# Kernel optimization log

Hardware: AMD Instinct MI355X
Metric: run time of the kernel (lower is better)

## Reference

```python
import jax, jax.numpy as jnp
import numpy as np

B, S, D, H = 2, 2048, 1024, 16
HD = D // H  # 64


def setup_inputs() -> dict:
    key = jax.random.key(0)
    ks = jax.random.split(key, 11)
    w_scale = 1.0 / np.sqrt(D)
    Q = jax.random.normal(ks[0], (B, S, D), jnp.float32)
    K = jax.random.normal(ks[1], (B, S, D), jnp.float32)
    V = jax.random.normal(ks[2], (B, S, D), jnp.float32)
    # causal mask: True = masked (matches torch masked_fill semantics)
    mask = ~jnp.tril(jnp.ones((S, S), bool))[None, None]  # [1,1,S,S]
    # RoPE freqs (precomputed cos/sin of freqs_cis, shape [S, HD//2])
    inv_freq = 1.0 / (10000.0 ** (jnp.arange(0, HD, 2, dtype=jnp.float32) / HD))
    angles = jnp.arange(S, dtype=jnp.float32)[:, None] * inv_freq[None, :]
    freqs_cos, freqs_sin = jnp.cos(angles), jnp.sin(angles)
    wq = jax.random.normal(ks[3], (D, D), jnp.float32) * w_scale
    wk = jax.random.normal(ks[4], (D, D), jnp.float32) * w_scale
    wv = jax.random.normal(ks[5], (D, D), jnp.float32) * w_scale
    wo = jax.random.normal(ks[6], (D, D), jnp.float32) * w_scale
    bq = jax.random.normal(ks[7], (D,), jnp.float32) * 0.01
    bk = jax.random.normal(ks[8], (D,), jnp.float32) * 0.01
    bv = jax.random.normal(ks[9], (D,), jnp.float32) * 0.01
    bo = jax.random.normal(ks[10], (D,), jnp.float32) * 0.01
    return {"Q": Q, "K": K, "V": V, "mask": mask,
            "freqs_cos": freqs_cos, "freqs_sin": freqs_sin,
            "wq": wq, "bq": bq, "wk": wk, "bk": bk,
            "wv": wv, "bv": bv, "wo": wo, "bo": bo}


def _rope(x, cos, sin):
    # x: [B,S,H,HD]; complex pairing of adjacent dims as in view_as_complex
    xr, xi = x[..., 0::2], x[..., 1::2]
    c = cos[None, :, None, :]
    s = sin[None, :, None, :]
    out_r = xr * c - xi * s
    out_i = xr * s + xi * c
    return jnp.stack([out_r, out_i], axis=-1).reshape(x.shape)


def reference(Q, K, V, mask, freqs_cos, freqs_sin, wq, bq, wk, bk, wv, bv, wo, bo):
    b, s, d = Q.shape
    h = H
    hd = d // h
    q = (Q @ wq.T + bq).reshape(b, s, h, hd)
    k = (K @ wk.T + bk).reshape(b, s, h, hd)
    v = (V @ wv.T + bv).reshape(b, s, h, hd)
    q = _rope(q, freqs_cos, freqs_sin)
    k = _rope(k, freqs_cos, freqs_sin)
    q = q.transpose(0, 2, 1, 3)  # [B,H,S,HD]
    k = k.transpose(0, 2, 1, 3)
    v = v.transpose(0, 2, 1, 3)
    scale = jnp.sqrt(jnp.float32(hd))
    energy = jnp.einsum('bhqd,bhkd->bhqk', q, k) / scale
    energy = jnp.where(mask, jnp.float32(-1e10), energy)
    attn = jax.nn.softmax(energy, axis=-1)  # dropout p=0.0 -> identity
    out = jnp.einsum('bhqk,bhkd->bhqd', attn, v)
    out = out.transpose(0, 2, 1, 3).reshape(b, s, d)
    return out @ wo.T + bo
```

## Files before the change

kernel.cpp:

```cpp
#include <hip/hip_runtime.h>
#include <stdint.h>

#define NB 2
#define NS 2048
#define ND 1024
#define NH 16
#define NHD 64
#define NM (NB*NS)

typedef __bf16 bf16;
typedef float f32x4 __attribute__((ext_vector_type(4)));
typedef __bf16 bf16x8 __attribute__((ext_vector_type(8)));
typedef __bf16 bf16x4 __attribute__((ext_vector_type(4)));

#define MFMA16(a,b,c) __builtin_amdgcn_mfma_f32_16x16x32_bf16(a,b,c,0,0,0)

__device__ __forceinline__ void gld_lds16(const bf16* g, bf16* l) {
  __builtin_amdgcn_global_load_lds((const __attribute__((address_space(1))) void*)g,
                                   (__attribute__((address_space(3))) void*)l,
                                   16, 0, 0);
}

__device__ __forceinline__ void block_sync_lds() {
  asm volatile("s_waitcnt lgkmcnt(0)\n\ts_barrier" ::: "memory");
}

__global__ __launch_bounds__(256)
void cvt3(const float* __restrict__ s0, const float* __restrict__ s1,
          const float* __restrict__ s2, bf16* __restrict__ dst, int n4each) {
  const int t = blockIdx.y;
  const float* s = (t == 0) ? s0 : (t == 1) ? s1 : s2;
  int i = blockIdx.x * blockDim.x + threadIdx.x;
  if (i >= n4each) return;
  float4 v = ((const float4*)s)[i];
  bf16x4 o = { (bf16)v.x, (bf16)v.y, (bf16)v.z, (bf16)v.w };
  ((bf16x4*)(dst + (size_t)t * n4each * 4))[i] = o;
}

__global__ __launch_bounds__(256)
void cvt_w4(const float* __restrict__ s0, const float* __restrict__ s1,
            const float* __restrict__ s2, const float* __restrict__ s3,
            bf16* __restrict__ dst, int n4each) {
  const int t = blockIdx.y;
  const float* s = (t == 0) ? s0 : (t == 1) ? s1 : (t == 2) ? s2 : s3;
  int i = blockIdx.x * blockDim.x + threadIdx.x;
  if (i >= n4each) return;
  float4 v = ((const float4*)s)[i];
  bf16x4 o = { (bf16)v.x, (bf16)v.y, (bf16)v.z, (bf16)v.w };
  ((bf16x4*)(dst + (size_t)t * n4each * 4))[i] = o;
}

template<int MODE>
__global__ __launch_bounds__(256)
void gemm_nt(const bf16* __restrict__ A, const bf16* __restrict__ W,
             const float* __restrict__ b0, const float* __restrict__ b1,
             const float* __restrict__ b2,
             const float* __restrict__ fc, const float* __restrict__ fs,
             bf16* __restrict__ obf, bf16* __restrict__ vtp,
             float* __restrict__ of) {
  constexpr int K = ND;
  constexpr int BN = (MODE == 0) ? 128 : 64;
  constexpr int NJ = (MODE == 0) ? 4 : 2;
  constexpr int ITB = (MODE == 0) ? 4 : 2;
  __shared__ __align__(16) bf16 As[128 * 64];
  __shared__ __align__(16) bf16 Bs[BN * 64];
  const int tid = threadIdx.x;
  const int w = tid >> 6, lane = tid & 63;

  const int id = blockIdx.x;
  const int xcd = id & 7, r = id >> 3;
  int t, nt, mt;
  if (MODE == 0) { t = r >> 5; const int rem = r & 31; nt = rem & 7;  mt = xcd + 8 * (rem >> 3); }
  else           { t = 0;                              nt = r & 15;   mt = xcd + 8 * (r >> 4);   }

  const bf16* Ab = A + (size_t)t * ((size_t)NM * K);
  const bf16* Wb = W + (size_t)t * ((size_t)ND * K);
  const float* bias = (t == 0) ? b0 : (t == 1) ? b1 : b2;
  const int wr = (w >> 1) * 64, wc = (w & 1) * (BN / 2);
  f32x4 acc[4][NJ] = {};

  const int swsrc = (((lane & 7) ^ ((lane >> 3) & 7)) << 3);
  const bf16* ga = Ab + (size_t)(mt * 128 + w * 8 + (lane >> 3)) * K + swsrc;
  const bf16* gb = Wb + (size_t)(nt * BN + w * 8 + (lane >> 3)) * K + swsrc;

  for (int k0 = 0; k0 < K; k0 += 64) {
    __syncthreads();
#pragma unroll
    for (int it = 0; it < 4; ++it)
      gld_lds16(ga + (size_t)(it * 32) * K + k0, As + (it * 4 + w) * 512);
#pragma unroll
    for (int it = 0; it < ITB; ++it)
      gld_lds16(gb + (size_t)(it * 32) * K + k0, Bs + (it * 4 + w) * 512);
    __syncthreads();

#pragma unroll
    for (int ks = 0; ks < 2; ++ks) {
      bf16x8 af[4], bfr[NJ];
#pragma unroll
      for (int i = 0; i < 4; ++i) {
        const int row = wr + i * 16 + (lane & 15);
        af[i] = *(const bf16x8*)&As[row * 64 +
                 (((ks * 4 + (lane >> 4)) ^ (lane & 7)) << 3)];
      }
#pragma unroll
      for (int j = 0; j < NJ; ++j) {
        const int row = wc + j * 16 + (lane & 15);
        bfr[j] = *(const bf16x8*)&Bs[row * 64 +
                  (((ks * 4 + (lane >> 4)) ^ (lane & 7)) << 3)];
      }
#pragma unroll
      for (int i = 0; i < 4; ++i)
#pragma unroll
        for (int j = 0; j < NJ; ++j)
          acc[i][j] = MFMA16(af[i], bfr[j], acc[i][j]);
    }
  }

#pragma unroll
  for (int i = 0; i < 4; ++i) {
#pragma unroll
    for (int j = 0; j < NJ; ++j) {
      const int gcol = nt * BN + wc + j * 16 + (lane & 15);
      const float bv = bias[gcol];
      if (MODE == 0 && t == 2) {
        const int s0g = mt * 128 + wr + i * 16 + (lane >> 4) * 4;
        const int b = s0g >> 11, s = s0g & (NS - 1);
        const int h = gcol >> 6, hd = gcol & 63;
        bf16x4 pk = { (bf16)(acc[i][j][0] + bv), (bf16)(acc[i][j][1] + bv),
                      (bf16)(acc[i][j][2] + bv), (bf16)(acc[i][j][3] + bv) };
        *(bf16x4*)&vtp[((size_t)(b * NH + h) * NHD + hd) * NS + s] = pk;
        continue;
      }
#pragma unroll
      for (int r4 = 0; r4 < 4; ++r4) {
        const int grow = mt * 128 + wr + i * 16 + (lane >> 4) * 4 + r4;
        float v = acc[i][j][r4] + bv;
        if (MODE == 0) {
          const int b = grow >> 11, s = grow & (NS - 1);
          const int h = gcol >> 6, hd = gcol & 63;
          float pv = __shfl_xor(v, 1);
          const int ii = hd >> 1;
          float c  = fc[(s << 5) + ii];
          float sn = fs[(s << 5) + ii];
          v = ((hd & 1) == 0) ? (v * c - pv * sn) : (pv * sn + v * c);
          if (t == 0) v *= 0.18033688011112042f;
          obf[(size_t)t * ((size_t)NM * ND) +
              (((size_t)(b * NH + h) * NS + s) * NHD + hd)] = (bf16)v;
        } else {
          of[(size_t)grow * ND + gcol] = v;
        }
      }
    }
  }
}

__device__ __forceinline__ void attn_tile(
    const bf16* __restrict__ Ksh, const bf16* __restrict__ Vsh,
    bf16* __restrict__ Pw, const bf16x8* qf, f32x4* o,
    float& m, float& l, int qi, int kk0, bool diag, int qrow, int grp) {
  const int s7 = qrow & 7;
  f32x4 sc[4] = {};
  __builtin_amdgcn_s_setprio(1);
#pragma unroll
  for (int ch = 0; ch < 2; ++ch)
#pragma unroll
    for (int cb = 0; cb < 4; ++cb) {
      bf16x8 kf = *(const bf16x8*)
        &Ksh[(cb * 16 + qrow) * 64 + (((ch * 4 + grp) ^ s7) << 3)];
      sc[cb] = MFMA16(kf, qf[ch], sc[cb]);
    }
  __builtin_amdgcn_s_setprio(0);

  if (diag) {
#pragma unroll
    for (int cb = 0; cb < 4; ++cb)
#pragma unroll
      for (int r = 0; r < 4; ++r)
        if (kk0 + cb * 16 + grp * 4 + r > qi) sc[cb][r] = -1e30f;
  }

  float a0 = fmaxf(fmaxf(sc[0][0], sc[0][1]), fmaxf(sc[0][2], sc[0][3]));
  float a1 = fmaxf(fmaxf(sc[1][0], sc[1][1]), fmaxf(sc[1][2], sc[1][3]));
  float a2 = fmaxf(fmaxf(sc[2][0], sc[2][1]), fmaxf(sc[2][2], sc[2][3]));
  float a3 = fmaxf(fmaxf(sc[3][0], sc[3][1]), fmaxf(sc[3][2], sc[3][3]));
  float pm = fmaxf(fmaxf(a0, a1), fmaxf(a2, a3));

  if (__any(pm > m + 8.f)) {
    float px = fmaxf(pm, __shfl_xor(pm, 16));
    px = fmaxf(px, __shfl_xor(px, 32));
    const float mn = fmaxf(m, px);
    const float scl = exp2f(m - mn);
    m = mn;
    l *= scl;
#pragma unroll
    for (int hb = 0; hb < 4; ++hb)
#pragma unroll
      for (int r = 0; r < 4; ++r) o[hb][r] *= scl;
  }

#pragma unroll
  for (int cb = 0; cb < 4; ++cb) {
    bf16x4 pk;
#pragma unroll
    for (int r = 0; r < 4; ++r) {
      float p = exp2f(sc[cb][r] - m);
      l += p;
      pk[r] = (bf16)p;
    }
    *(bf16x4*)&Pw[qrow * 64 + (((((cb << 1) | (grp >> 1)) ^ s7) << 3)) +
                  ((grp & 1) << 2)] = pk;
  }

  __builtin_amdgcn_s_setprio(1);
#pragma unroll
  for (int ch = 0; ch < 2; ++ch) {
    bf16x8 pa = *(const bf16x8*)
      &Pw[qrow * 64 + (((ch * 4 + grp) ^ s7) << 3)];
#pragma unroll
    for (int hb = 0; hb < 4; ++hb) {
      bf16x8 vf = *(const bf16x8*)
        &Vsh[(hb * 16 + qrow) * 64 + (((ch * 4 + grp) ^ s7) << 3)];
      o[hb] = MFMA16(vf, pa, o[hb]);
    }
  }
  __builtin_amdgcn_s_setprio(0);
}

__global__ __launch_bounds__(512, 4)
void attn_k(const bf16* __restrict__ q, const bf16* __restrict__ k,
            const bf16* __restrict__ vt, bf16* __restrict__ out) {
  __shared__ __align__(16) char smem[81920];
  bf16* KV = (bf16*)smem;
  bf16* Pr = (bf16*)(smem + 65536);
  auto MO = (float(*)[2][16][68])smem;
  auto ML = (float(*)[2][16][2])(smem + 36864);

  const int tid = threadIdx.x;
  const int w = tid >> 6, lane = tid & 63;
  const int h = w >> 2, wl = w & 3;
  const int qrow = lane & 15, grp = lane >> 4;
  const int bh = blockIdx.x, j = blockIdx.y;
  const int b = bh >> 4, hh = bh & (NH - 1);
  const int tA = j, tB = 31 - j;

  const bf16* qb = q + (size_t)bh * NS * NHD;
  const bf16* kb = k + (size_t)bh * NS * NHD;
  const bf16* vb = vt + (size_t)bh * NHD * NS;

  const int nA = (j >= h) ? (((j - h) >> 1) + 1) : 0;
  const int nB = (((31 - j) - h) >> 1) + 1;
  const int len = nA + nB;

  const int q0A = tA * 64 + wl * 16, q0B = tB * 64 + wl * 16;
  bf16x8 qfA[2], qfB[2];
#pragma unroll
  for (int ch = 0; ch < 2; ++ch) {
    qfA[ch] = *(const bf16x8*)&qb[(size_t)(q0A + qrow) * NHD + ch * 32 + grp * 8];
    qfB[ch] = *(const bf16x8*)&qb[(size_t)(q0B + qrow) * NHD + ch * 32 + grp * 8];
  }

  f32x4 oA[4] = {}, oB[4] = {};
  float mA = -1e30f, lA = 0.f, mB = -1e30f, lB = 0.f;

  const int local = tid & 255;
  const int r0 = local >> 3;
  const int c0 = (local & 7) * 8;
  const int sw = (((local & 7) ^ (r0 & 7)) << 3);

  bf16* Pw = Pr + w * 1024;
  auto Kb = [&](int buf) { return KV + ((h * 2 + buf) * 2 + 0) * 4096; };
  auto Vb = [&](int buf) { return KV + ((h * 2 + buf) * 2 + 1) * 4096; };

  bf16x8 ka0, ka1, va0, va1;
  auto load_round = [&](int r) {
    const bool isA = r < nA;
    const int kt = isA ? (h + 2 * r) : (h + 2 * (r - nA));
    const int kk0 = kt * 64;
    ka0 = *(const bf16x8*)&kb[(size_t)(kk0 + r0) * NHD + c0];
    ka1 = *(const bf16x8*)&kb[(size_t)(kk0 + r0 + 32) * NHD + c0];
    va0 = *(const bf16x8*)&vb[(size_t)r0 * NS + kk0 + c0];
    va1 = *(const bf16x8*)&vb[(size_t)(r0 + 32) * NS + kk0 + c0];
  };
  auto store_tile = [&](int buf) {
    bf16* Ksc = Kb(buf);
    bf16* Vsc = Vb(buf);
    *(bf16x8*)&Ksc[r0 * 64 + sw]        = ka0;
    *(bf16x8*)&Ksc[(r0 + 32) * 64 + sw] = ka1;
    *(bf16x8*)&Vsc[r0 * 64 + sw]        = va0;
    *(bf16x8*)&Vsc[(r0 + 32) * 64 + sw] = va1;
  };

  load_round(0);
  store_tile(0);
  load_round(1);
  block_sync_lds();

  for (int r = 0; r < 17; ++r) {
    const int cur = r & 1;
    const bool act = r < len;
    if (r + 1 < len) store_tile(cur ^ 1);
    if (r + 2 < len) load_round(r + 2);
    if (act) {
      const bool isA = r < nA;
      const int kt = isA ? (h + 2 * r) : (h + 2 * (r - nA));
      if (isA)
        attn_tile(Kb(cur), Vb(cur), Pw, qfA, oA, mA, lA,
                  q0A + qrow, kt * 64, kt == tA, qrow, grp);
      else
        attn_tile(Kb(cur), Vb(cur), Pw, qfB, oB, mB, lB,
                  q0B + qrow, kt * 64, kt == tB, qrow, grp);
    }
    block_sync_lds();
  }

  lA += __shfl_xor(lA, 16); lA += __shfl_xor(lA, 32);
  lB += __shfl_xor(lB, 16); lB += __shfl_xor(lB, 32);

  __syncthreads();

  if (h == 1) {
#pragma unroll
    for (int hb = 0; hb < 4; ++hb) {
      *(f32x4*)&MO[wl][0][qrow][hb * 16 + grp * 4] = oA[hb];
      *(f32x4*)&MO[wl][1][qrow][hb * 16 + grp * 4] = oB[hb];
    }
    if (grp == 0) {
      ML[wl][0][qrow][0] = mA; ML[wl][0][qrow][1] = lA;
      ML[wl][1][qrow][0] = mB; ML[wl][1][qrow][1] = lB;
    }
  }
  __syncthreads();

  if (h == 0) {
#pragma unroll
    for (int sub = 0; sub < 2; ++sub) {
      const float m0 = sub ? mB : mA, l0 = sub ? lB : lA;
      const f32x4* o0 = sub ? oB : oA;
      const float m1 = ML[wl][sub][qrow][0], l1 = ML[wl][sub][qrow][1];
      const float mm = fmaxf(m0, m1);
      const float s0 = exp2f(m0 - mm), s1 = exp2f(m1 - mm);
      const float inv = 1.f / (l0 * s0 + l1 * s1);
      const int s = (sub ? q0B : q0A) + qrow;
      bf16* op = out + (size_t)(b * NS + s) * ND + hh * NHD + grp * 4;
#pragma unroll
      for (int hb = 0; hb < 4; ++hb) {
        f32x4 o1 = *(const f32x4*)&MO[wl][sub][qrow][hb * 16 + grp * 4];
        bf16x4 ov = { (bf16)((o0[hb][0] * s0 + o1[0] * s1) * inv),
                      (bf16)((o0[hb][1] * s0 + o1[1] * s1) * inv),
                      (bf16)((o0[hb][2] * s0 + o1[2] * s1) * inv),
                      (bf16)((o0[hb][3] * s0 + o1[3] * s1) * inv) };
        *(bf16x4*)&op[hb * 16] = ov;
      }
    }
  }
}

extern "C" void kernel_launch(void* const* d_in, const int* in_sizes, int n_in,
                              void* d_out, int out_size, void* d_ws, size_t ws_size,
                              hipStream_t stream) {
  const float* Q  = (const float*)d_in[0];
  const float* K  = (const float*)d_in[1];
  const float* V  = (const float*)d_in[2];
  const float* fc = (const float*)d_in[4];
  const float* fs = (const float*)d_in[5];
  const float* wq = (const float*)d_in[6];
  const float* bq = (const float*)d_in[7];
  const float* wk = (const float*)d_in[8];
  const float* bk = (const float*)d_in[9];
  const float* wv = (const float*)d_in[10];
  const float* bv = (const float*)d_in[11];
  const float* wo = (const float*)d_in[12];
  const float* bo = (const float*)d_in[13];
  float* out = (float*)d_out;
  bf16* ws = (bf16*)d_ws;

  const size_t MB_ = 1024 * 1024;
  bf16* Qbf  = ws;
  bf16* Wqkv = ws + 12 * MB_;
  bf16* Wo   = ws + 15 * MB_;
  bf16* qp   = ws + 16 * MB_;
  bf16* kp   = ws + 20 * MB_;
  bf16* vtp  = ws + 28 * MB_;
  bf16* aout = ws + 32 * MB_;

  cvt3<<<dim3(4096, 3), 256, 0, stream>>>(Q, K, V, Qbf, 1048576);
  cvt_w4<<<dim3(1024, 4), 256, 0, stream>>>(wq, wk, wv, wo, Wqkv, 262144);

  gemm_nt<0><<<768, 256, 0, stream>>>(Qbf, Wqkv, bq, bk, bv, fc, fs,
                                      qp, vtp, nullptr);

  attn_k<<<dim3(32, 16), 512, 0, stream>>>(qp, kp, vtp, aout);

  gemm_nt<1><<<512, 256, 0, stream>>>(aout, Wo, bo, bo, bo, fc, fs,
                                      nullptr, nullptr, out);
}
```

Baseline: 122.2 us.

## Share K/V tiles across paired query tiles in one 256-thread attention block

Restructures the causal attention kernel so that a 4-wave block walks every key tile once. Each K tile in LDS is used for both the early (tA) and late (tB) query tile, replacing the old 8-wave split-KV scheme and its final LDS merge of partial softmax states. It also fuses the two fp32-to-bf16 conversion kernels into a single launch. The trade-off is a longer serial loop per block (up to 32 rounds) and fewer waves per block, with less parallelism inside each block.

```diff
diff --git a/kernel.cpp b/kernel.cpp
--- a/kernel.cpp
+++ b/kernel.cpp
@@ -26,28 +26,20 @@
 }
 
 __global__ __launch_bounds__(256)
-void cvt3(const float* __restrict__ s0, const float* __restrict__ s1,
-          const float* __restrict__ s2, bf16* __restrict__ dst, int n4each) {
+void cvt7(const float* __restrict__ s0, const float* __restrict__ s1,
+          const float* __restrict__ s2, const float* __restrict__ s3,
+          const float* __restrict__ s4, const float* __restrict__ s5,
+          const float* __restrict__ s6, bf16* __restrict__ dst) {
   const int t = blockIdx.y;
-  const float* s = (t == 0) ? s0 : (t == 1) ? s1 : s2;
+  const float* s = (t == 0) ? s0 : (t == 1) ? s1 : (t == 2) ? s2 :
+                   (t == 3) ? s3 : (t == 4) ? s4 : (t == 5) ? s5 : s6;
+  const int n4 = (t < 3) ? (1 << 20) : (1 << 18);
+  const size_t eoff = (t < 3) ? ((size_t)t << 22) : ((size_t)12 << 20) + ((size_t)(t - 3) << 20);
   int i = blockIdx.x * blockDim.x + threadIdx.x;
-  if (i >= n4each) return;
+  if (i >= n4) return;
   float4 v = ((const float4*)s)[i];
   bf16x4 o = { (bf16)v.x, (bf16)v.y, (bf16)v.z, (bf16)v.w };
-  ((bf16x4*)(dst + (size_t)t * n4each * 4))[i] = o;
-}
-
-__global__ __launch_bounds__(256)
-void cvt_w4(const float* __restrict__ s0, const float* __restrict__ s1,
-            const float* __restrict__ s2, const float* __restrict__ s3,
-            bf16* __restrict__ dst, int n4each) {
-  const int t = blockIdx.y;
-  const float* s = (t == 0) ? s0 : (t == 1) ? s1 : (t == 2) ? s2 : s3;
-  int i = blockIdx.x * blockDim.x + threadIdx.x;
-  if (i >= n4each) return;
-  float4 v = ((const float4*)s)[i];
-  bf16x4 o = { (bf16)v.x, (bf16)v.y, (bf16)v.z, (bf16)v.w };
-  ((bf16x4*)(dst + (size_t)t * n4each * 4))[i] = o;
+  ((bf16x4*)(dst + eoff))[i] = o;
 }
 
 template<int MODE>
@@ -154,31 +146,10 @@
   }
 }
 
-__device__ __forceinline__ void attn_tile(
-    const bf16* __restrict__ Ksh, const bf16* __restrict__ Vsh,
-    bf16* __restrict__ Pw, const bf16x8* qf, f32x4* o,
-    float& m, float& l, int qi, int kk0, bool diag, int qrow, int grp) {
+__device__ __forceinline__ void softmax_pv(
+    f32x4* sc, bf16* __restrict__ Pw, const bf16* __restrict__ Vsh,
+    f32x4* o, float& m, float& l, int qrow, int grp) {
   const int s7 = qrow & 7;
-  f32x4 sc[4] = {};
-  __builtin_amdgcn_s_setprio(1);
-#pragma unroll
-  for (int ch = 0; ch < 2; ++ch)
-#pragma unroll
-    for (int cb = 0; cb < 4; ++cb) {
-      bf16x8 kf = *(const bf16x8*)
-        &Ksh[(cb * 16 + qrow) * 64 + (((ch * 4 + grp) ^ s7) << 3)];
-      sc[cb] = MFMA16(kf, qf[ch], sc[cb]);
-    }
-  __builtin_amdgcn_s_setprio(0);
-
-  if (diag) {
-#pragma unroll
-    for (int cb = 0; cb < 4; ++cb)
-#pragma unroll
-      for (int r = 0; r < 4; ++r)
-        if (kk0 + cb * 16 + grp * 4 + r > qi) sc[cb][r] = -1e30f;
-  }
-
   float a0 = fmaxf(fmaxf(sc[0][0], sc[0][1]), fmaxf(sc[0][2], sc[0][3]));
   float a1 = fmaxf(fmaxf(sc[1][0], sc[1][1]), fmaxf(sc[1][2], sc[1][3]));
   float a2 = fmaxf(fmaxf(sc[2][0], sc[2][1]), fmaxf(sc[2][2], sc[2][3]));
@@ -214,8 +185,7 @@
   __builtin_amdgcn_s_setprio(1);
 #pragma unroll
   for (int ch = 0; ch < 2; ++ch) {
-    bf16x8 pa = *(const bf16x8*)
-      &Pw[qrow * 64 + (((ch * 4 + grp) ^ s7) << 3)];
+    bf16x8 pa = *(const bf16x8*)&Pw[qrow * 64 + (((ch * 4 + grp) ^ s7) << 3)];
 #pragma unroll
     for (int hb = 0; hb < 4; ++hb) {
       bf16x8 vf = *(const bf16x8*)
@@ -226,32 +196,26 @@
   __builtin_amdgcn_s_setprio(0);
 }
 
-__global__ __launch_bounds__(512, 4)
+__global__ __launch_bounds__(256, 4)
 void attn_k(const bf16* __restrict__ q, const bf16* __restrict__ k,
             const bf16* __restrict__ vt, bf16* __restrict__ out) {
-  __shared__ __align__(16) char smem[81920];
-  bf16* KV = (bf16*)smem;
-  bf16* Pr = (bf16*)(smem + 65536);
-  auto MO = (float(*)[2][16][68])smem;
-  auto ML = (float(*)[2][16][2])(smem + 36864);
+  __shared__ __align__(16) bf16 Ks[2][4096];
+  __shared__ __align__(16) bf16 Vs[2][4096];
+  __shared__ __align__(16) bf16 Pr[4][1024];
 
   const int tid = threadIdx.x;
   const int w = tid >> 6, lane = tid & 63;
-  const int h = w >> 2, wl = w & 3;
   const int qrow = lane & 15, grp = lane >> 4;
   const int bh = blockIdx.x, j = blockIdx.y;
   const int b = bh >> 4, hh = bh & (NH - 1);
   const int tA = j, tB = 31 - j;
+  const int nrounds = tB + 1;
 
   const bf16* qb = q + (size_t)bh * NS * NHD;
   const bf16* kb = k + (size_t)bh * NS * NHD;
   const bf16* vb = vt + (size_t)bh * NHD * NS;
 
-  const int nA = (j >= h) ? (((j - h) >> 1) + 1) : 0;
-  const int nB = (((31 - j) - h) >> 1) + 1;
-  const int len = nA + nB;
-
-  const int q0A = tA * 64 + wl * 16, q0B = tB * 64 + wl * 16;
+  const int q0A = tA * 64 + w * 16, q0B = tB * 64 + w * 16;
   bf16x8 qfA[2], qfB[2];
 #pragma unroll
   for (int ch = 0; ch < 2; ++ch) {
@@ -262,32 +226,25 @@
   f32x4 oA[4] = {}, oB[4] = {};
   float mA = -1e30f, lA = 0.f, mB = -1e30f, lB = 0.f;
 
-  const int local = tid & 255;
-  const int r0 = local >> 3;
-  const int c0 = (local & 7) * 8;
-  const int sw = (((local & 7) ^ (r0 & 7)) << 3);
-
-  bf16* Pw = Pr + w * 1024;
-  auto Kb = [&](int buf) { return KV + ((h * 2 + buf) * 2 + 0) * 4096; };
-  auto Vb = [&](int buf) { return KV + ((h * 2 + buf) * 2 + 1) * 4096; };
+  const int r0 = tid >> 3;
+  const int c0 = (tid & 7) * 8;
+  const int sw = (((tid & 7) ^ (r0 & 7)) << 3);
+
+  bf16* Pw = Pr[w];
 
   bf16x8 ka0, ka1, va0, va1;
   auto load_round = [&](int r) {
-    const bool isA = r < nA;
-    const int kt = isA ? (h + 2 * r) : (h + 2 * (r - nA));
-    const int kk0 = kt * 64;
+    const int kk0 = r * 64;
     ka0 = *(const bf16x8*)&kb[(size_t)(kk0 + r0) * NHD + c0];
     ka1 = *(const bf16x8*)&kb[(size_t)(kk0 + r0 + 32) * NHD + c0];
     va0 = *(const bf16x8*)&vb[(size_t)r0 * NS + kk0 + c0];
     va1 = *(const bf16x8*)&vb[(size_t)(r0 + 32) * NS + kk0 + c0];
   };
   auto store_tile = [&](int buf) {
-    bf16* Ksc = Kb(buf);
-    bf16* Vsc = Vb(buf);
-    *(bf16x8*)&Ksc[r0 * 64 + sw]        = ka0;
-    *(bf16x8*)&Ksc[(r0 + 32) * 64 + sw] = ka1;
-    *(bf16x8*)&Vsc[r0 * 64 + sw]        = va0;
-    *(bf16x8*)&Vsc[(r0 + 32) * 64 + sw] = va1;
+    *(bf16x8*)&Ks[buf][r0 * 64 + sw]        = ka0;
+    *(bf16x8*)&Ks[buf][(r0 + 32) * 64 + sw] = ka1;
+    *(bf16x8*)&Vs[buf][r0 * 64 + sw]        = va0;
+    *(bf16x8*)&Vs[buf][(r0 + 32) * 64 + sw] = va1;
   };
 
   load_round(0);
@@ -295,62 +252,74 @@
   load_round(1);
   block_sync_lds();
 
-  for (int r = 0; r < 17; ++r) {
+  for (int r = 0; r < nrounds; ++r) {
     const int cur = r & 1;
-    const bool act = r < len;
-    if (r + 1 < len) store_tile(cur ^ 1);
-    if (r + 2 < len) load_round(r + 2);
-    if (act) {
-      const bool isA = r < nA;
-      const int kt = isA ? (h + 2 * r) : (h + 2 * (r - nA));
-      if (isA)
-        attn_tile(Kb(cur), Vb(cur), Pw, qfA, oA, mA, lA,
-                  q0A + qrow, kt * 64, kt == tA, qrow, grp);
-      else
-        attn_tile(Kb(cur), Vb(cur), Pw, qfB, oB, mB, lB,
-                  q0B + qrow, kt * 64, kt == tB, qrow, grp);
-    }
+    if (r + 1 < nrounds) store_tile(cur ^ 1);
+    if (r + 2 < nrounds) load_round(r + 2);
+
+    const bool dual = (r <= tA);
+    const int s7 = qrow & 7;
+    f32x4 sA[4] = {}, sB[4] = {};
+    __builtin_amdgcn_s_setprio(1);
+#pragma unroll
+    for (int ch = 0; ch < 2; ++ch)
+#pragma unroll
+      for (int cb = 0; cb < 4; ++cb) {
+        bf16x8 kf = *(const bf16x8*)
+          &Ks[cur][(cb * 16 + qrow) * 64 + (((ch * 4 + grp) ^ s7) << 3)];
+        sB[cb] = MFMA16(kf, qfB[ch], sB[cb]);
+        if (dual) sA[cb] = MFMA16(kf, qfA[ch], sA[cb]);
+      }
+    __builtin_amdgcn_s_setprio(0);
+
+    const int kk0 = r * 64;
+    if (r == tB) {
+      const int qi = q0B + qrow;
+#pragma unroll
+      for (int cb = 0; cb < 4; ++cb)
+#pragma unroll
+        for (int rr = 0; rr < 4; ++rr)
+          if (kk0 + cb * 16 + grp * 4 + rr > qi) sB[cb][rr] = -1e30f;
+    }
+    softmax_pv(sB, Pw, Vs[cur], oB, mB, lB, qrow, grp);
+
+    if (dual) {
+      if (r == tA) {
+        const int qi = q0A + qrow;
+#pragma unroll
+        for (int cb = 0; cb < 4; ++cb)
+#pragma unroll
+          for (int rr = 0; rr < 4; ++rr)
+            if (kk0 + cb * 16 + grp * 4 + rr > qi) sA[cb][rr] = -1e30f;
+      }
+      softmax_pv(sA, Pw, Vs[cur], oA, mA, lA, qrow, grp);
+    }
+
     block_sync_lds();
   }
 
   lA += __shfl_xor(lA, 16); lA += __shfl_xor(lA, 32);
   lB += __shfl_xor(lB, 16); lB += __shfl_xor(lB, 32);
-
-  __syncthreads();
-
-  if (h == 1) {
+  {
+    const float inv = 1.f / lB;
+    const int s = q0B + qrow;
+    bf16* op = out + (size_t)(b * NS + s) * ND + hh * NHD + grp * 4;
 #pragma unroll
     for (int hb = 0; hb < 4; ++hb) {
-      *(f32x4*)&MO[wl][0][qrow][hb * 16 + grp * 4] = oA[hb];
-      *(f32x4*)&MO[wl][1][qrow][hb * 16 + grp * 4] = oB[hb];
-    }
-    if (grp == 0) {
-      ML[wl][0][qrow][0] = mA; ML[wl][0][qrow][1] = lA;
-      ML[wl][1][qrow][0] = mB; ML[wl][1][qrow][1] = lB;
-    }
-  }
-  __syncthreads();
-
-  if (h == 0) {
-#pragma unroll
-    for (int sub = 0; sub < 2; ++sub) {
-      const float m0 = sub ? mB : mA, l0 = sub ? lB : lA;
-      const f32x4* o0 = sub ? oB : oA;
-      const float m1 = ML[wl][sub][qrow][0], l1 = ML[wl][sub][qrow][1];
-      const float mm = fmaxf(m0, m1);
-      const float s0 = exp2f(m0 - mm), s1 = exp2f(m1 - mm);
-      const float inv = 1.f / (l0 * s0 + l1 * s1);
-      const int s = (sub ? q0B : q0A) + qrow;
-      bf16* op = out + (size_t)(b * NS + s) * ND + hh * NHD + grp * 4;
-#pragma unroll
-      for (int hb = 0; hb < 4; ++hb) {
-        f32x4 o1 = *(const f32x4*)&MO[wl][sub][qrow][hb * 16 + grp * 4];
-        bf16x4 ov = { (bf16)((o0[hb][0] * s0 + o1[0] * s1) * inv),
-                      (bf16)((o0[hb][1] * s0 + o1[1] * s1) * inv),
-                      (bf16)((o0[hb][2] * s0 + o1[2] * s1) * inv),
-                      (bf16)((o0[hb][3] * s0 + o1[3] * s1) * inv) };
-        *(bf16x4*)&op[hb * 16] = ov;
-      }
+      bf16x4 ov = { (bf16)(oB[hb][0] * inv), (bf16)(oB[hb][1] * inv),
+                    (bf16)(oB[hb][2] * inv), (bf16)(oB[hb][3] * inv) };
+      *(bf16x4*)&op[hb * 16] = ov;
+    }
+  }
+  {
+    const float inv = 1.f / lA;
+    const int s = q0A + qrow;
+    bf16* op = out + (size_t)(b * NS + s) * ND + hh * NHD + grp * 4;
+#pragma unroll
+    for (int hb = 0; hb < 4; ++hb) {
+      bf16x4 ov = { (bf16)(oA[hb][0] * inv), (bf16)(oA[hb][1] * inv),
+                    (bf16)(oA[hb][2] * inv), (bf16)(oA[hb][3] * inv) };
+      *(bf16x4*)&op[hb * 16] = ov;
     }
   }
 }
@@ -383,13 +352,12 @@
   bf16* vtp  = ws + 28 * MB_;
   bf16* aout = ws + 32 * MB_;
 
-  cvt3<<<dim3(4096, 3), 256, 0, stream>>>(Q, K, V, Qbf, 1048576);
-  cvt_w4<<<dim3(1024, 4), 256, 0, stream>>>(wq, wk, wv, wo, Wqkv, 262144);
+  cvt7<<<dim3(4096, 7), 256, 0, stream>>>(Q, K, V, wq, wk, wv, wo, ws);
 
   gemm_nt<0><<<768, 256, 0, stream>>>(Qbf, Wqkv, bq, bk, bv, fc, fs,
                                       qp, vtp, nullptr);
 
-  attn_k<<<dim3(32, 16), 512, 0, stream>>>(qp, kp, vtp, aout);
+  attn_k<<<dim3(32, 16), 256, 0, stream>>>(qp, kp, vtp, aout);
 
   gemm_nt<1><<<512, 256, 0, stream>>>(aout, Wo, bo, bo, bo, fc, fs,
                                       nullptr, nullptr, out);
```

After: 245.4 us. 101% more time.

## Fuse fp32-to-bf16 activation conversion into QKV GEMM and shrink GEMM tiles

Applied to the files above, without the earlier changes.

Removes the separate cvt3 kernel: the QKV projection now reads fp32 Q/K/V directly, converts them to bf16 in registers and writes the swizzled tile to LDS itself. This drops a full fp32 read plus bf16 write and re-read of the activations. The QKV GEMM tile shrinks from 128x128 to 128x64, and the output projection gets its own 64x64 kernel, launching more blocks. The cost is synchronous register-staged A loads instead of the async global-to-LDS path, and more redundant reads of A and W across the smaller tiles.

```diff
diff --git a/kernel.cpp b/kernel.cpp
--- a/kernel.cpp
+++ b/kernel.cpp
@@ -23,18 +23,6 @@
 
 __device__ __forceinline__ void block_sync_lds() {
   asm volatile("s_waitcnt lgkmcnt(0)\n\ts_barrier" ::: "memory");
-}
-
-__global__ __launch_bounds__(256)
-void cvt3(const float* __restrict__ s0, const float* __restrict__ s1,
-          const float* __restrict__ s2, bf16* __restrict__ dst, int n4each) {
-  const int t = blockIdx.y;
-  const float* s = (t == 0) ? s0 : (t == 1) ? s1 : s2;
-  int i = blockIdx.x * blockDim.x + threadIdx.x;
-  if (i >= n4each) return;
-  float4 v = ((const float4*)s)[i];
-  bf16x4 o = { (bf16)v.x, (bf16)v.y, (bf16)v.z, (bf16)v.w };
-  ((bf16x4*)(dst + (size_t)t * n4each * 4))[i] = o;
 }
 
 __global__ __launch_bounds__(256)
@@ -50,52 +38,57 @@
   ((bf16x4*)(dst + (size_t)t * n4each * 4))[i] = o;
 }
 
-template<int MODE>
 __global__ __launch_bounds__(256)
-void gemm_nt(const bf16* __restrict__ A, const bf16* __restrict__ W,
-             const float* __restrict__ b0, const float* __restrict__ b1,
-             const float* __restrict__ b2,
-             const float* __restrict__ fc, const float* __restrict__ fs,
-             bf16* __restrict__ obf, bf16* __restrict__ vtp,
-             float* __restrict__ of) {
+void gemm_qkv(const float* __restrict__ Qf, const float* __restrict__ Kf,
+              const float* __restrict__ Vf, const bf16* __restrict__ W,
+              const float* __restrict__ b0, const float* __restrict__ b1,
+              const float* __restrict__ b2,
+              const float* __restrict__ fc, const float* __restrict__ fs,
+              bf16* __restrict__ obf, bf16* __restrict__ vtp) {
   constexpr int K = ND;
-  constexpr int BN = (MODE == 0) ? 128 : 64;
-  constexpr int NJ = (MODE == 0) ? 4 : 2;
-  constexpr int ITB = (MODE == 0) ? 4 : 2;
   __shared__ __align__(16) bf16 As[128 * 64];
-  __shared__ __align__(16) bf16 Bs[BN * 64];
+  __shared__ __align__(16) bf16 Bs[64 * 64];
   const int tid = threadIdx.x;
   const int w = tid >> 6, lane = tid & 63;
 
   const int id = blockIdx.x;
   const int xcd = id & 7, r = id >> 3;
-  int t, nt, mt;
-  if (MODE == 0) { t = r >> 5; const int rem = r & 31; nt = rem & 7;  mt = xcd + 8 * (rem >> 3); }
-  else           { t = 0;                              nt = r & 15;   mt = xcd + 8 * (r >> 4);   }
-
-  const bf16* Ab = A + (size_t)t * ((size_t)NM * K);
+  const int t = r >> 6;
+  const int rem = r & 63;
+  const int nt = rem & 15;
+  const int mt = xcd + 8 * (rem >> 4);
+
+  const float* Ab = (t == 0) ? Qf : (t == 1) ? Kf : Vf;
   const bf16* Wb = W + (size_t)t * ((size_t)ND * K);
   const float* bias = (t == 0) ? b0 : (t == 1) ? b1 : b2;
-  const int wr = (w >> 1) * 64, wc = (w & 1) * (BN / 2);
-  f32x4 acc[4][NJ] = {};
-
-  const int swsrc = (((lane & 7) ^ ((lane >> 3) & 7)) << 3);
-  const bf16* ga = Ab + (size_t)(mt * 128 + w * 8 + (lane >> 3)) * K + swsrc;
-  const bf16* gb = Wb + (size_t)(nt * BN + w * 8 + (lane >> 3)) * K + swsrc;
+  const int wr = (w >> 1) * 64, wc = (w & 1) * 32;
+  f32x4 acc[4][2] = {};
+
+  const int srow = w * 8 + (lane >> 3);
+  const int scol = (lane & 7) * 8;
+  const int swz  = (((lane & 7) ^ ((lane >> 3) & 7)) << 3);
+  const float* ga = Ab + (size_t)(mt * 128 + srow) * K + scol;
+  const bf16* gb = Wb + (size_t)(nt * 64 + srow) * K + swz;
 
   for (int k0 = 0; k0 < K; k0 += 64) {
     __syncthreads();
 #pragma unroll
-    for (int it = 0; it < 4; ++it)
-      gld_lds16(ga + (size_t)(it * 32) * K + k0, As + (it * 4 + w) * 512);
-#pragma unroll
-    for (int it = 0; it < ITB; ++it)
+    for (int it = 0; it < 2; ++it)
       gld_lds16(gb + (size_t)(it * 32) * K + k0, Bs + (it * 4 + w) * 512);
+#pragma unroll
+    for (int it = 0; it < 4; ++it) {
+      const float* p = ga + (size_t)(it * 32) * K + k0;
+      float4 f0 = *(const float4*)p;
+      float4 f1 = *(const float4*)(p + 4);
+      bf16x8 v8 = { (bf16)f0.x, (bf16)f0.y, (bf16)f0.z, (bf16)f0.w,
+                    (bf16)f1.x, (bf16)f1.y, (bf16)f1.z, (bf16)f1.w };
+      *(bf16x8*)&As[(it * 32 + srow) * 64 + swz] = v8;
+    }
     __syncthreads();
 
 #pragma unroll
     for (int ks = 0; ks < 2; ++ks) {
-      bf16x8 af[4], bfr[NJ];
+      bf16x8 af[4], bfr[2];
 #pragma unroll
       for (int i = 0; i < 4; ++i) {
         const int row = wr + i * 16 + (lane & 15);
@@ -103,7 +96,7 @@
                  (((ks * 4 + (lane >> 4)) ^ (lane & 7)) << 3)];
       }
 #pragma unroll
-      for (int j = 0; j < NJ; ++j) {
+      for (int j = 0; j < 2; ++j) {
         const int row = wc + j * 16 + (lane & 15);
         bfr[j] = *(const bf16x8*)&Bs[row * 64 +
                   (((ks * 4 + (lane >> 4)) ^ (lane & 7)) << 3)];
@@ -111,7 +104,7 @@
 #pragma unroll
       for (int i = 0; i < 4; ++i)
 #pragma unroll
-        for (int j = 0; j < NJ; ++j)
+        for (int j = 0; j < 2; ++j)
           acc[i][j] = MFMA16(af[i], bfr[j], acc[i][j]);
     }
   }
@@ -119,10 +112,10 @@
 #pragma unroll
   for (int i = 0; i < 4; ++i) {
 #pragma unroll
-    for (int j = 0; j < NJ; ++j) {
-      const int gcol = nt * BN + wc + j * 16 + (lane & 15);
+    for (int j = 0; j < 2; ++j) {
+      const int gcol = nt * 64 + wc + j * 16 + (lane & 15);
       const float bv = bias[gcol];
-      if (MODE == 0 && t == 2) {
+      if (t == 2) {
         const int s0g = mt * 128 + wr + i * 16 + (lane >> 4) * 4;
         const int b = s0g >> 11, s = s0g & (NS - 1);
         const int h = gcol >> 6, hd = gcol & 63;
@@ -135,20 +128,85 @@
       for (int r4 = 0; r4 < 4; ++r4) {
         const int grow = mt * 128 + wr + i * 16 + (lane >> 4) * 4 + r4;
         float v = acc[i][j][r4] + bv;
-        if (MODE == 0) {
-          const int b = grow >> 11, s = grow & (NS - 1);
-          const int h = gcol >> 6, hd = gcol & 63;
-          float pv = __shfl_xor(v, 1);
-          const int ii = hd >> 1;
-          float c  = fc[(s << 5) + ii];
-          float sn = fs[(s << 5) + ii];
-          v = ((hd & 1) == 0) ? (v * c - pv * sn) : (pv * sn + v * c);
-          if (t == 0) v *= 0.18033688011112042f;
-          obf[(size_t)t * ((size_t)NM * ND) +
-              (((size_t)(b * NH + h) * NS + s) * NHD + hd)] = (bf16)v;
-        } else {
-          of[(size_t)grow * ND + gcol] = v;
-        }
+        const int b = grow >> 11, s = grow & (NS - 1);
+        const int h = gcol >> 6, hd = gcol & 63;
+        float pv = __shfl_xor(v, 1);
+        const int ii = hd >> 1;
+        float c  = fc[(s << 5) + ii];
+        float sn = fs[(s << 5) + ii];
+        v = ((hd & 1) == 0) ? (v * c - pv * sn) : (pv * sn + v * c);
+        if (t == 0) v *= 0.18033688011112042f;
+        obf[(size_t)t * ((size_t)NM * ND) +
+            (((size_t)(b * NH + h) * NS + s) * NHD + hd)] = (bf16)v;
+      }
+    }
+  }
+}
+
+__global__ __launch_bounds__(256)
+void gemm_out(const bf16* __restrict__ A, const bf16* __restrict__ W,
+              const float* __restrict__ b0, float* __restrict__ of) {
+  constexpr int K = ND;
+  __shared__ __align__(16) bf16 As[64 * 64];
+  __shared__ __align__(16) bf16 Bs[64 * 64];
+  const int tid = threadIdx.x;
+  const int w = tid >> 6, lane = tid & 63;
+
+  const int id = blockIdx.x;
+  const int xcd = id & 7, r = id >> 3;
+  const int nt = r & 15;
+  const int mt = xcd + 8 * (r >> 4);
+
+  const int wr = (w >> 1) * 32, wc = (w & 1) * 32;
+  f32x4 acc[2][2] = {};
+
+  const int swsrc = (((lane & 7) ^ ((lane >> 3) & 7)) << 3);
+  const bf16* ga = A + (size_t)(mt * 64 + w * 8 + (lane >> 3)) * K + swsrc;
+  const bf16* gb = W + (size_t)(nt * 64 + w * 8 + (lane >> 3)) * K + swsrc;
+
+  for (int k0 = 0; k0 < K; k0 += 64) {
+    __syncthreads();
+#pragma unroll
+    for (int it = 0; it < 2; ++it)
+      gld_lds16(ga + (size_t)(it * 32) * K + k0, As + (it * 4 + w) * 512);
+#pragma unroll
+    for (int it = 0; it < 2; ++it)
+      gld_lds16(gb + (size_t)(it * 32) * K + k0, Bs + (it * 4 + w) * 512);
+    __syncthreads();
+
+#pragma unroll
+    for (int ks = 0; ks < 2; ++ks) {
+      bf16x8 af[2], bfr[2];
+#pragma unroll
+      for (int i = 0; i < 2; ++i) {
+        const int row = wr + i * 16 + (lane & 15);
+        af[i] = *(const bf16x8*)&As[row * 64 +
+                 (((ks * 4 + (lane >> 4)) ^ (lane & 7)) << 3)];
+      }
+#pragma unroll
+      for (int j = 0; j < 2; ++j) {
+        const int row = wc + j * 16 + (lane & 15);
+        bfr[j] = *(const bf16x8*)&Bs[row * 64 +
+                  (((ks * 4 + (lane >> 4)) ^ (lane & 7)) << 3)];
+      }
+#pragma unroll
+      for (int i = 0; i < 2; ++i)
+#pragma unroll
+        for (int j = 0; j < 2; ++j)
+          acc[i][j] = MFMA16(af[i], bfr[j], acc[i][j]);
+    }
+  }
+
+#pragma unroll
+  for (int i = 0; i < 2; ++i) {
+#pragma unroll
+    for (int j = 0; j < 2; ++j) {
+      const int gcol = nt * 64 + wc + j * 16 + (lane & 15);
+      const float bv = b0[gcol];
+#pragma unroll
+      for (int r4 = 0; r4 < 4; ++r4) {
+        const int grow = mt * 64 + wr + i * 16 + (lane >> 4) * 4 + r4;
+        of[(size_t)grow * ND + gcol] = acc[i][j][r4] + bv;
       }
     }
   }
@@ -375,7 +433,6 @@
   bf16* ws = (bf16*)d_ws;
 
   const size_t MB_ = 1024 * 1024;
-  bf16* Qbf  = ws;
   bf16* Wqkv = ws + 12 * MB_;
   bf16* Wo   = ws + 15 * MB_;
   bf16* qp   = ws + 16 * MB_;
@@ -383,14 +440,12 @@
   bf16* vtp  = ws + 28 * MB_;
   bf16* aout = ws + 32 * MB_;
 
-  cvt3<<<dim3(4096, 3), 256, 0, stream>>>(Q, K, V, Qbf, 1048576);
   cvt_w4<<<dim3(1024, 4), 256, 0, stream>>>(wq, wk, wv, wo, Wqkv, 262144);
 
-  gemm_nt<0><<<768, 256, 0, stream>>>(Qbf, Wqkv, bq, bk, bv, fc, fs,
-                                      qp, vtp, nullptr);
+  gemm_qkv<<<1536, 256, 0, stream>>>(Q, K, V, Wqkv, bq, bk, bv, fc, fs,
+                                     qp, vtp);
 
   attn_k<<<dim3(32, 16), 512, 0, stream>>>(qp, kp, vtp, aout);
 
-  gemm_nt<1><<<512, 256, 0, stream>>>(aout, Wo, bo, bo, bo, fc, fs,
-                                      nullptr, nullptr, out);
-}
+  gemm_out<<<1024, 256, 0, stream>>>(aout, Wo, bo, out);
+}
```

New measurement: 120.5 us. Within noise of the previous version (-1.4%).
